# Kernel tuning notes

Measured on AMD Instinct MI355X. Metric: run time of the kernel, lower is better.

## Reference

```python
import jax, jax.numpy as jnp
import numpy as np

BETA = 0.5
CODEBOOK_STD = 0.02


def setup_inputs() -> dict:
    key = jax.random.key(0)
    k1, k2 = jax.random.split(key)
    x = jax.random.normal(k1, (16, 4096, 128), dtype=jnp.float32)
    codebook = CODEBOOK_STD * jax.random.normal(k2, (4096, 128), dtype=jnp.float32)
    return {"x": x, "codebook": codebook}


def reference(x, codebook):
    """SharedVectorQuantizer.forward (eval): tokens, STE-quantized, vq_loss.

    x:        [B, N, D] float
    codebook: [K, D]    float (embedding.weight)
    """
    B, N, D = x.shape
    flat_x = x.reshape(-1, D)  # [B*N, D]
    # Squared euclidean distances; argmin equals torch.cdist argmin.
    # d2[i,k] = ||x_i||^2 - 2 x_i . e_k + ||e_k||^2
    d2 = (
        jnp.sum(flat_x * flat_x, axis=-1, keepdims=True)
        - 2.0 * (flat_x @ codebook.T)
        + jnp.sum(codebook * codebook, axis=-1)
    )  # [B*N, K]
    tokens_flat = jnp.argmin(d2, axis=1)  # [B*N] int
    tokens = tokens_flat.reshape(B, N)
    quantized = codebook[tokens]  # [B, N, D] embedding gather

    # Losses (MSE with mean reduction)
    commitment_loss = jnp.mean((jax.lax.stop_gradient(quantized) - x) ** 2)
    embedding_loss = jnp.mean((quantized - jax.lax.stop_gradient(x)) ** 2)
    vq_loss = embedding_loss + BETA * commitment_loss

    # Straight-through estimator
    quantized_ste = x + jax.lax.stop_gradient(quantized - x)
    return tokens, quantized_ste, vq_loss
```

## Files before the change

kernel.cpp:

```cpp
#include <hip/hip_runtime.h>


#define D_ 128
#define MROWS 65536
#define KCODES 4096
#define NSUB 16
#define SUBCAP 512

#define OQ_AH    4194304
#define OQ_KEYS  4456448
#define OQ_PAIRS 4587520
#define OQ_T1    5111808
#define OQ_T3    5177344
#define OQ_CNT   5181440
#define OQ_T3HL  5197824

typedef __attribute__((ext_vector_type(8))) short bf16x8;
typedef __attribute__((ext_vector_type(16))) float f32x16;

__device__ __forceinline__ unsigned short bf16rne(float f) {
  unsigned u = __float_as_uint(f);
  unsigned r = (u + 0x7FFFu + ((u >> 16) & 1u)) >> 16;
  return (unsigned short)r;
}
__device__ __forceinline__ float bf16tof(unsigned short h) {
  return __uint_as_float(((unsigned)h) << 16);
}

__device__ __forceinline__ void gload_lds16(const void* g, void* l) {
  __builtin_amdgcn_global_load_lds(
      (const __attribute__((address_space(1))) unsigned int*)g,
      (__attribute__((address_space(3))) unsigned int*)l, 16, 0, 0);
}

__device__ __forceinline__ float4 f4add(float4 a, float4 b) {
  return make_float4(a.x + b.x, a.y + b.y, a.z + b.z, a.w + b.w);
}
__device__ __forceinline__ float4 f4sq(float4 v) {
  return make_float4(v.x * v.x, v.y * v.y, v.z * v.z, v.w * v.w);
}

__device__ __forceinline__ float np_sumsq_row(const float4* __restrict__ r) {
  float4 W[4];
#pragma unroll
  for (int a = 0; a < 4; ++a) {
    float4 c0 = f4sq(r[0 * 4 + a]), c1 = f4sq(r[1 * 4 + a]);
    float4 c2 = f4sq(r[2 * 4 + a]), c3 = f4sq(r[3 * 4 + a]);
    float4 c4 = f4sq(r[4 * 4 + a]), c5 = f4sq(r[5 * 4 + a]);
    float4 c6 = f4sq(r[6 * 4 + a]), c7 = f4sq(r[7 * 4 + a]);
    W[a] = f4add(f4add(f4add(c0, c1), f4add(c2, c3)),
                 f4add(f4add(c4, c5), f4add(c6, c7)));
  }
  float4 U0 = f4add(W[0], W[2]);
  float4 U1 = f4add(W[1], W[3]);
  float4 T = f4add(U0, U1);
  float s0 = T.x + T.z, s1 = T.y + T.w;
  return s0 + s1;
}

__global__ __launch_bounds__(256, 2)
void k_pre(const float* __restrict__ x, const float* __restrict__ cb,
           float* __restrict__ outq) {
  int gid = blockIdx.x * 256 + threadIdx.x;
  float* t1 = outq + OQ_T1;
  float* t3 = outq + OQ_T3;
  unsigned* t3hl = (unsigned*)(outq + OQ_T3HL);
  int* cnt = (int*)(outq + OQ_CNT);

  t1[gid] = np_sumsq_row((const float4*)(x + (size_t)gid * D_));
  if (gid < KCODES) {
    float s = np_sumsq_row((const float4*)(cb + (size_t)gid * D_));
    t3[gid] = s;
    unsigned short h = bf16rne(s);
    unsigned short l = bf16rne(s - bf16tof(h));
    t3hl[gid] = (unsigned)h | ((unsigned)l << 16);
  }
  if (gid < 64 * NSUB * 16) cnt[gid] = 0;

  int u = gid;
  int ch = u >> 10, r = u & 1023;
  int s2 = r >> 6, p = r & 63;
  int kt = s2 >> 1, ct = s2 & 1;
  int kg = p >> 5, nl = p & 31;
  int code = ch * 64 + ct * 32 + nl;
  const float* src = cb + (size_t)code * D_ + (kt * 2 + kg) * 8;
  bf16x8 h8;
#pragma unroll
  for (int e = 0; e < 8; ++e) h8[e] = (short)bf16rne(src[e]);
  *(bf16x8*)((char*)(outq + OQ_AH) + (size_t)u * 16) = h8;
}

__global__ __launch_bounds__(256, 3)
void k_big(const float* __restrict__ x, const unsigned* __restrict__ t3hl,
           float* __restrict__ outq) {
  __shared__ char lds[2][16384];
  const int tid = threadIdx.x;
  const int lane = tid & 63;
  const int w = tid >> 6;
  const int kg = lane >> 5, nl = lane & 31;
  const int rb = blockIdx.x >> 2, cs = blockIdx.x & 3;
  const int row0 = rb * 256 + w * 64;

  const char* AhB = (const char*)(outq + OQ_AH);
  float* cm = outq;

  bf16x8 xh[2][8];
#pragma unroll
  for (int xt = 0; xt < 2; ++xt)
#pragma unroll
    for (int kt = 0; kt < 8; ++kt) {
      const float* src =
          x + (size_t)(row0 + xt * 32 + nl) * D_ + (kt * 2 + kg) * 8;
      float f[8];
      *(float4*)(f) = *(const float4*)(src);
      *(float4*)(f + 4) = *(const float4*)(src + 4);
      bf16x8 h;
#pragma unroll
      for (int e = 0; e < 8; ++e) h[e] = (short)bf16rne(f[e]);
      xh[xt][kt] = h;
    }

  bf16x8 bneg = 0;
  if (kg == 0) { bneg[0] = (short)0xBF00; bneg[1] = (short)0xBF00; }

#define STAGE(c, buf)                                                         \
  {                                                                           \
    const char* sAh = AhB + (size_t)(c) * 16384;                              \
    _Pragma("unroll")                                                         \
    for (int i4 = 0; i4 < 4; ++i4) {                                          \
      int ub = i4 * 256 + w * 64;                                             \
      gload_lds16(sAh + (size_t)(ub + lane) * 16, (buf) + ub * 16);           \
    }                                                                         \
  }

  STAGE(cs * 16 + 0, lds[0]);
  __syncthreads();

  int b = 0;
  for (int it = 0; it < 16; ++it) {
    int ch = cs * 16 + it;
    char* cur = lds[b];
    if (it < 15) STAGE(ch + 1, lds[b ^ 1]);

    unsigned v0 = t3hl[ch * 64 + nl];
    unsigned v1 = t3hl[ch * 64 + 32 + nl];
    bf16x8 s0 = 0, s1 = 0;
    if (kg == 0) {
      s0[0] = (short)(v0 & 0xFFFFu); s0[1] = (short)(v0 >> 16);
      s1[0] = (short)(v1 & 0xFFFFu); s1[1] = (short)(v1 >> 16);
    }

    f32x16 a00 = 0, a01 = 0, a10 = 0, a11 = 0;
    a00 = __builtin_amdgcn_mfma_f32_32x32x16_bf16(s0, bneg, a00, 0, 0, 0);
    a01 = __builtin_amdgcn_mfma_f32_32x32x16_bf16(s0, bneg, a01, 0, 0, 0);
    a10 = __builtin_amdgcn_mfma_f32_32x32x16_bf16(s1, bneg, a10, 0, 0, 0);
    a11 = __builtin_amdgcn_mfma_f32_32x32x16_bf16(s1, bneg, a11, 0, 0, 0);
#pragma unroll
    for (int kt = 0; kt < 8; ++kt) {
      bf16x8 e0 = *(const bf16x8*)(cur + ((kt * 2 + 0) * 64 + lane) * 16);
      bf16x8 e1 = *(const bf16x8*)(cur + ((kt * 2 + 1) * 64 + lane) * 16);
      a00 = __builtin_amdgcn_mfma_f32_32x32x16_bf16(e0, xh[0][kt], a00, 0, 0, 0);
      a01 = __builtin_amdgcn_mfma_f32_32x32x16_bf16(e0, xh[1][kt], a01, 0, 0, 0);
      a10 = __builtin_amdgcn_mfma_f32_32x32x16_bf16(e1, xh[0][kt], a10, 0, 0, 0);
      a11 = __builtin_amdgcn_mfma_f32_32x32x16_bf16(e1, xh[1][kt], a11, 0, 0, 0);
    }

    float m0 = -3.4e38f, m1 = -3.4e38f;
#pragma unroll
    for (int e = 0; e < 16; ++e) {
      m0 = fmaxf(m0, fmaxf(a00[e], a10[e]));
      m1 = fmaxf(m1, fmaxf(a01[e], a11[e]));
    }
    m0 = fmaxf(m0, __shfl_xor(m0, 32, 64));
    m1 = fmaxf(m1, __shfl_xor(m1, 32, 64));
    float mv = (kg == 0) ? m0 : m1;
    cm[(size_t)ch * MROWS + row0 + kg * 32 + nl] = mv;
    __syncthreads();
    b ^= 1;
  }
#undef STAGE
}

__global__ __launch_bounds__(256, 4)
void k_cand(const float* __restrict__ cm, int* __restrict__ cnt,
            int* __restrict__ pairs, unsigned long long* __restrict__ keys,
            float dlt) {
  __shared__ float wmax[4][64];
  __shared__ float thrs[64];
  const int tid = threadIdx.x, lane = tid & 63, w = tid >> 6;
  const int r = blockIdx.x * 64 + lane;
  const int sub = blockIdx.x & (NSUB - 1);
  float v[16];
#pragma unroll
  for (int i = 0; i < 16; ++i) v[i] = cm[(size_t)(w * 16 + i) * MROWS + r];
  float m = v[0];
#pragma unroll
  for (int i = 1; i < 16; ++i) m = fmaxf(m, v[i]);
  wmax[w][lane] = m;
  __syncthreads();
  if (w == 0) {
    float A = fmaxf(fmaxf(wmax[0][lane], wmax[1][lane]),
                    fmaxf(wmax[2][lane], wmax[3][lane]));
    thrs[lane] = A - dlt;
    keys[r] = ~0ull;
  }
  __syncthreads();
  float thr = thrs[lane];
#pragma unroll
  for (int i = 0; i < 16; ++i) {
    if (v[i] >= thr) {
      int ch = w * 16 + i;
      int slot = ch * NSUB + sub;
      int s = atomicAdd(cnt + slot * 16, 1);
      if (s < SUBCAP) pairs[slot * SUBCAP + s] = r;
    }
  }
}

__global__ __launch_bounds__(256, 2)
void k_exact(const float* __restrict__ x, const float* __restrict__ cb,
             const int* __restrict__ cnt, const int* __restrict__ pairs,
             const float* __restrict__ t1, const float* __restrict__ t3,
             unsigned long long* __restrict__ keys) {
  __shared__ float elds[32 * 65 * 4];
  __shared__ float xlds[4][D_];
  int ch = blockIdx.x >> 4, sub = blockIdx.x & (NSUB - 1);
  int tid = threadIdx.x, lane = tid & 63, wid = tid >> 6;
#pragma unroll
  for (int it2 = 0; it2 < 8; ++it2) {
    int u = it2 * 256 + tid;
    int c = u >> 5, d4 = u & 31;
    float4 v = *(const float4*)(cb + ((size_t)ch * 64 + c) * D_ + d4 * 4);
    *(float4*)(elds + (d4 * 65 + c) * 4) = v;
  }
  float t3v = t3[ch * 64 + lane];
  __syncthreads();
  int slot = ch * NSUB + sub;
  int n = cnt[slot * 16]; if (n > SUBCAP) n = SUBCAP;
  const int* lst = pairs + slot * SUBCAP;
  for (int idx = wid; idx < n; idx += 4) {
    int row = lst[idx];
    *(float2*)(&xlds[wid][lane * 2]) = *(const float2*)(x + (size_t)row * D_ + lane * 2);
    asm volatile("s_waitcnt lgkmcnt(0)" ::: "memory");
    float acc = 0.f;
    float t1r = t1[row];
#pragma unroll 8
    for (int d4 = 0; d4 < 32; ++d4) {
      float4 xv = *(const float4*)(&xlds[wid][d4 * 4]);
      float4 ev = *(const float4*)(elds + (d4 * 65 + lane) * 4);
      acc = __builtin_fmaf(xv.x, ev.x, acc);
      acc = __builtin_fmaf(xv.y, ev.y, acc);
      acc = __builtin_fmaf(xv.z, ev.z, acc);
      acc = __builtin_fmaf(xv.w, ev.w, acc);
    }
    float s = __builtin_fmaf(-2.f, acc, t1r) + t3v;
    unsigned u32 = __float_as_uint(s);
    u32 = u32 ^ (unsigned)(((int)u32 >> 31) | 0x80000000);
    unsigned long long key =
        ((unsigned long long)u32 << 12) | (unsigned)(ch * 64 + lane);
#pragma unroll
    for (int off = 1; off < 64; off <<= 1) {
      unsigned long long o = __shfl_xor(key, off, 64);
      key = o < key ? o : key;
    }
    if (lane == 0) atomicMin(keys + row, key);
  }
}

__global__ __launch_bounds__(256, 2)
void k_final(const unsigned long long* __restrict__ keys,
             float* __restrict__ tok_f, int* __restrict__ tok_i) {
  int r = blockIdx.x * 256 + threadIdx.x;
  int code = (int)(keys[r] & 0xFFFull);
  tok_f[r] = (float)code;
  tok_i[r] = code;
}

__global__ __launch_bounds__(256, 2)
void k_gather(const float* __restrict__ x, const float* __restrict__ cb,
              const int* __restrict__ tok_i, float* __restrict__ outq,
              float* __restrict__ partial) {
  int idx = blockIdx.x * 256 + threadIdx.x;
  int row = idx >> 5;
  int d4 = idx & 31;
  int t = tok_i[row];
  float4 q = ((const float4*)(cb + (size_t)t * D_))[d4];
  float4 xv = ((const float4*)x)[idx];
  ((float4*)outq)[idx] = q;
  float dx = q.x - xv.x, dy = q.y - xv.y, dz = q.z - xv.z, dw = q.w - xv.w;
  float s = dx * dx + dy * dy + dz * dz + dw * dw;
#pragma unroll
  for (int off = 1; off < 64; off <<= 1) s += __shfl_xor(s, off, 64);
  __shared__ float red[4];
  int lane = threadIdx.x & 63, w = threadIdx.x >> 6;
  if (lane == 0) red[w] = s;
  __syncthreads();
  if (threadIdx.x == 0)
    partial[blockIdx.x] = red[0] + red[1] + red[2] + red[3];
}

__global__ __launch_bounds__(256, 1)
void k_loss(const float* __restrict__ partial, float* __restrict__ out_loss,
            float scale) {
  int i = blockIdx.x * 256 + threadIdx.x;
  float s = partial[i];
#pragma unroll
  for (int off = 1; off < 64; off <<= 1) s += __shfl_xor(s, off, 64);
  __shared__ float red[4];
  int lane = threadIdx.x & 63, w = threadIdx.x >> 6;
  if (lane == 0) red[w] = s;
  __syncthreads();
  if (threadIdx.x == 0)
    atomicAdd(out_loss, (red[0] + red[1] + red[2] + red[3]) * scale);
}

extern "C" void kernel_launch(void* const* d_in, const int* in_sizes, int n_in,
                              void* d_out, int out_size, void* d_ws, size_t ws_size,
                              hipStream_t stream) {
  const float* x = (const float*)d_in[0];
  const float* cb = (const float*)d_in[1];

  float* out_tok = (float*)d_out;
  float* outq = (float*)d_out + MROWS;
  float* out_loss = (float*)d_out + MROWS + (size_t)MROWS * D_;

  int* tok_i = (int*)d_ws;
  float* part = (float*)((char*)d_ws + 262144);

  float* t3 = outq + OQ_T3;
  float* t1 = outq + OQ_T1;
  unsigned* t3hl = (unsigned*)(outq + OQ_T3HL);
  int* cnt = (int*)(outq + OQ_CNT);
  int* pairs = (int*)(outq + OQ_PAIRS);
  unsigned long long* keys = (unsigned long long*)(outq + OQ_KEYS);

  k_pre<<<MROWS / 256, 256, 0, stream>>>(x, cb, outq);
  hipMemsetAsync(out_loss, 0, sizeof(float), stream);
  k_big<<<(MROWS / 256) * 4, 256, 0, stream>>>(x, t3hl, outq);
  k_cand<<<MROWS / 64, 256, 0, stream>>>(outq, cnt, pairs, keys, 8e-3f);
  k_exact<<<64 * NSUB, 256, 0, stream>>>(x, cb, cnt, pairs, t1, t3, keys);
  k_final<<<MROWS / 256, 256, 0, stream>>>(keys, out_tok, tok_i);
  const int gB = (MROWS * (D_ / 4)) / 256;
  k_gather<<<gB, 256, 0, stream>>>(x, cb, tok_i, outq, part);
  k_loss<<<32, 256, 0, stream>>>(part, out_loss,
                                 1.5f / (float)((size_t)MROWS * D_));
}
```

Measured before the change: 190.7 us.

## Split k_big code tile across wave pairs to halve accumulators and raise occupancy

Each wave in k_big now handles one 32-code half of the 64-code chunk for 64 rows, instead of the full chunk for 64 rows. Two waves share a row group, and their per-row maxima are combined through shared memory before one of them writes. This halves the accumulator registers per wave, which allows launch bounds of 4 blocks per SM and twice the blocks. In exchange, every codebook chunk is staged once per 128 rows instead of once per 256, which doubles LDS staging traffic, and each iteration adds an extra barrier and shared-memory exchange.

```diff
diff --git a/kernel.cpp b/kernel.cpp
--- a/kernel.cpp
+++ b/kernel.cpp
@@ -90,16 +90,18 @@
   *(bf16x8*)((char*)(outq + OQ_AH) + (size_t)u * 16) = h8;
 }
 
-__global__ __launch_bounds__(256, 3)
+__global__ __launch_bounds__(256, 4)
 void k_big(const float* __restrict__ x, const unsigned* __restrict__ t3hl,
            float* __restrict__ outq) {
   __shared__ char lds[2][16384];
+  __shared__ float comb[4][64];
   const int tid = threadIdx.x;
   const int lane = tid & 63;
-  const int w = tid >> 6;
+  const int wid = tid >> 6;
+  const int rg = wid >> 1, cth = wid & 1;
   const int kg = lane >> 5, nl = lane & 31;
   const int rb = blockIdx.x >> 2, cs = blockIdx.x & 3;
-  const int row0 = rb * 256 + w * 64;
+  const int rowb = rb * 128 + rg * 64;
 
   const char* AhB = (const char*)(outq + OQ_AH);
   float* cm = outq;
@@ -110,7 +112,7 @@
 #pragma unroll
     for (int kt = 0; kt < 8; ++kt) {
       const float* src =
-          x + (size_t)(row0 + xt * 32 + nl) * D_ + (kt * 2 + kg) * 8;
+          x + (size_t)(rowb + xt * 32 + nl) * D_ + (kt * 2 + kg) * 8;
       float f[8];
       *(float4*)(f) = *(const float4*)(src);
       *(float4*)(f + 4) = *(const float4*)(src + 4);
@@ -128,7 +130,7 @@
     const char* sAh = AhB + (size_t)(c) * 16384;                              \
     _Pragma("unroll")                                                         \
     for (int i4 = 0; i4 < 4; ++i4) {                                          \
-      int ub = i4 * 256 + w * 64;                                             \
+      int ub = i4 * 256 + wid * 64;                                           \
       gload_lds16(sAh + (size_t)(ub + lane) * 16, (buf) + ub * 16);           \
     }                                                                         \
   }
@@ -142,39 +144,39 @@
     char* cur = lds[b];
     if (it < 15) STAGE(ch + 1, lds[b ^ 1]);
 
-    unsigned v0 = t3hl[ch * 64 + nl];
-    unsigned v1 = t3hl[ch * 64 + 32 + nl];
-    bf16x8 s0 = 0, s1 = 0;
+    unsigned v = t3hl[ch * 64 + cth * 32 + nl];
+    bf16x8 sfrag = 0;
     if (kg == 0) {
-      s0[0] = (short)(v0 & 0xFFFFu); s0[1] = (short)(v0 >> 16);
-      s1[0] = (short)(v1 & 0xFFFFu); s1[1] = (short)(v1 >> 16);
-    }
-
-    f32x16 a00 = 0, a01 = 0, a10 = 0, a11 = 0;
-    a00 = __builtin_amdgcn_mfma_f32_32x32x16_bf16(s0, bneg, a00, 0, 0, 0);
-    a01 = __builtin_amdgcn_mfma_f32_32x32x16_bf16(s0, bneg, a01, 0, 0, 0);
-    a10 = __builtin_amdgcn_mfma_f32_32x32x16_bf16(s1, bneg, a10, 0, 0, 0);
-    a11 = __builtin_amdgcn_mfma_f32_32x32x16_bf16(s1, bneg, a11, 0, 0, 0);
+      sfrag[0] = (short)(v & 0xFFFFu);
+      sfrag[1] = (short)(v >> 16);
+    }
+
+    f32x16 a0 = 0, a1 = 0;
+    a0 = __builtin_amdgcn_mfma_f32_32x32x16_bf16(sfrag, bneg, a0, 0, 0, 0);
+    a1 = __builtin_amdgcn_mfma_f32_32x32x16_bf16(sfrag, bneg, a1, 0, 0, 0);
 #pragma unroll
     for (int kt = 0; kt < 8; ++kt) {
-      bf16x8 e0 = *(const bf16x8*)(cur + ((kt * 2 + 0) * 64 + lane) * 16);
-      bf16x8 e1 = *(const bf16x8*)(cur + ((kt * 2 + 1) * 64 + lane) * 16);
-      a00 = __builtin_amdgcn_mfma_f32_32x32x16_bf16(e0, xh[0][kt], a00, 0, 0, 0);
-      a01 = __builtin_amdgcn_mfma_f32_32x32x16_bf16(e0, xh[1][kt], a01, 0, 0, 0);
-      a10 = __builtin_amdgcn_mfma_f32_32x32x16_bf16(e1, xh[0][kt], a10, 0, 0, 0);
-      a11 = __builtin_amdgcn_mfma_f32_32x32x16_bf16(e1, xh[1][kt], a11, 0, 0, 0);
+      bf16x8 e0 = *(const bf16x8*)(cur + ((kt * 2 + cth) * 64 + lane) * 16);
+      a0 = __builtin_amdgcn_mfma_f32_32x32x16_bf16(e0, xh[0][kt], a0, 0, 0, 0);
+      a1 = __builtin_amdgcn_mfma_f32_32x32x16_bf16(e0, xh[1][kt], a1, 0, 0, 0);
     }
 
     float m0 = -3.4e38f, m1 = -3.4e38f;
 #pragma unroll
     for (int e = 0; e < 16; ++e) {
-      m0 = fmaxf(m0, fmaxf(a00[e], a10[e]));
-      m1 = fmaxf(m1, fmaxf(a01[e], a11[e]));
+      m0 = fmaxf(m0, a0[e]);
+      m1 = fmaxf(m1, a1[e]);
     }
     m0 = fmaxf(m0, __shfl_xor(m0, 32, 64));
     m1 = fmaxf(m1, __shfl_xor(m1, 32, 64));
     float mv = (kg == 0) ? m0 : m1;
-    cm[(size_t)ch * MROWS + row0 + kg * 32 + nl] = mv;
+
+    comb[wid][lane] = mv;
+    __syncthreads();
+    if (cth == 0) {
+      float o = comb[wid ^ 1][lane];
+      cm[(size_t)ch * MROWS + rowb + lane] = fmaxf(mv, o);
+    }
     __syncthreads();
     b ^= 1;
   }
@@ -336,7 +338,7 @@
 
   k_pre<<<MROWS / 256, 256, 0, stream>>>(x, cb, outq);
   hipMemsetAsync(out_loss, 0, sizeof(float), stream);
-  k_big<<<(MROWS / 256) * 4, 256, 0, stream>>>(x, t3hl, outq);
+  k_big<<<(MROWS / 128) * 4, 256, 0, stream>>>(x, t3hl, outq);
   k_cand<<<MROWS / 64, 256, 0, stream>>>(outq, cnt, pairs, keys, 8e-3f);
   k_exact<<<64 * NSUB, 256, 0, stream>>>(x, cb, cnt, pairs, t1, t3, keys);
   k_final<<<MROWS / 256, 256, 0, stream>>>(keys, out_tok, tok_i);
```

Result: slower. 203.9 us (+6.9%).
